# Kernel tuning notes

Measured on AMD Instinct MI355X. Metric: run time of the kernel, lower is better.

Reference implementation:

```python
import jax, jax.numpy as jnp
import numpy as np

B, S, D, H, DFF = 4, 1024, 1024, 16, 4096
DK = D // H
EPS = 1e-6


def setup_inputs() -> dict:
    key = jax.random.key(0)
    ks = jax.random.split(key, 16)
    sd = 0.02
    inp = {
        "x_v": jax.random.normal(ks[0], (B, S, D), jnp.float32),
        "x_k": jax.random.normal(ks[1], (B, S, D), jnp.float32),
        "x_q": jax.random.normal(ks[2], (B, S, D), jnp.float32),
        "mask": jnp.zeros((B, 1, S), jnp.float32),
        # per-head projections stacked: [H, D, DK]
        "wq": jax.random.normal(ks[3], (H, D, DK), jnp.float32) * sd,
        "bq": jnp.zeros((H, DK), jnp.float32),
        "wk": jax.random.normal(ks[4], (H, D, DK), jnp.float32) * sd,
        "bk": jnp.zeros((H, DK), jnp.float32),
        "wv": jax.random.normal(ks[5], (H, D, DK), jnp.float32) * sd,
        "bv": jnp.zeros((H, DK), jnp.float32),
        "w0": jax.random.normal(ks[6], (D, D), jnp.float32) * sd,
        "b0": jnp.zeros((D,), jnp.float32),
        "ln1_g": jnp.ones((D,), jnp.float32),
        "ln1_b": jnp.zeros((D,), jnp.float32),
        "ff1_w": jax.random.normal(ks[7], (D, DFF), jnp.float32) * sd,
        "ff1_b": jnp.zeros((DFF,), jnp.float32),
        "ff2_w": jax.random.normal(ks[8], (DFF, D), jnp.float32) * sd,
        "ff2_b": jnp.zeros((D,), jnp.float32),
        "ln2_g": jnp.ones((D,), jnp.float32),
        "ln2_b": jnp.zeros((D,), jnp.float32),
    }
    return inp


def layer_norm(x, g, b):
    mu = jnp.mean(x, axis=-1, keepdims=True)
    var = jnp.mean(jnp.square(x - mu), axis=-1, keepdims=True)
    return (x - mu) * jax.lax.rsqrt(var + EPS) * g + b


def reference(x_v, x_k, x_q, mask, wq, bq, wk, bk, wv, bv, w0, b0,
              ln1_g, ln1_b, ff1_w, ff1_b, ff2_w, ff2_b, ln2_g, ln2_b):
    # --- Multi-head attention (heads batched instead of Python loop) ---
    q = jnp.einsum('bsd,hdk->bhsk', x_q, wq) + bq[:, None, :]  # [B,H,S,DK]
    k = jnp.einsum('bsd,hdk->bhsk', x_k, wk) + bk[:, None, :]
    v = jnp.einsum('bsd,hdk->bhsk', x_v, wv) + bv[:, None, :]
    scores = jnp.einsum('bhqk,bhsk->bhqs', q, k) / jnp.sqrt(jnp.float32(DK))
    scores = scores + mask[:, None, :, :] * (-1e9)  # mask broadcast over heads
    attn_w = jax.nn.softmax(scores, axis=-1)        # [B,H,S,S]
    attn = jnp.einsum('bhqs,bhsk->bhqk', attn_w, v)  # [B,H,S,DK]
    concat = attn.transpose(0, 2, 1, 3).reshape(B, S, D)
    mha_out = concat @ w0 + b0
    # --- Residual + LayerNorm 1 (dropout is identity at inference) ---
    sub1 = layer_norm(x_q + mha_out, ln1_g, ln1_b)
    # --- Point-wise FFN ---
    ffn = jax.nn.relu(sub1 @ ff1_w + ff1_b) @ ff2_w + ff2_b
    # --- Residual + LayerNorm 2 ---
    out = layer_norm(sub1 + ffn, ln2_g, ln2_b)
    # original returns the attention weights of the LAST head only
    return out, attn_w[:, -1]
```

## Files before the change

kernel.cpp:

```cpp
#include <hip/hip_runtime.h>
#include <hip/hip_bf16.h>
#include <stdint.h>

#define DEV __device__ __forceinline__

typedef uint16_t u16;
typedef __attribute__((ext_vector_type(8))) short s16x8;
typedef __attribute__((ext_vector_type(8))) unsigned short u16x8;
typedef __attribute__((ext_vector_type(4))) unsigned short u16x4;
typedef __attribute__((ext_vector_type(4))) float f32x4;

constexpr int CB = 4;
constexpr int CS = 1024;
constexpr int CD = 1024;
constexpr int CH = 16;
constexpr int CDFF = 4096;
constexpr int KVB = 128;
constexpr int LSTRP = 136;
constexpr float QSCALE = 0.125f * 1.44269504f;
constexpr float MASKC  = -1.44269504e9f;

DEV float b2f(u16 u) { union { uint32_t i; float f; } v; v.i = (uint32_t)u << 16; return v.f; }
DEV u16 f2b(float f) {
  union { float f; uint32_t i; } v; v.f = f;
  uint32_t r = v.i + 0x7fffu + ((v.i >> 16) & 1u);
  return (u16)(r >> 16);
}
DEV float ex2(float x) {
#if __has_builtin(__builtin_amdgcn_exp2f)
  return __builtin_amdgcn_exp2f(x);
#else
  return __expf(x * 0.69314718056f);
#endif
}

using as1v = const __attribute__((address_space(1))) void;
using as3v = __attribute__((address_space(3))) void;
DEV void g2l16(const u16* g, u16* l) {
  __builtin_amdgcn_global_load_lds((as1v*)g, (as3v*)l, 16, 0, 0);
}

__global__ void detect_dtype(const uint32_t* __restrict__ w, uint32_t* __restrict__ flag) {
  if (threadIdx.x == 0 && blockIdx.x == 0) {
    flag[0] = (w[0] == 0x3F800000u) ? 1u : 0u;
    flag[1] = 0u;
  }
}

__global__ __launch_bounds__(256)
void cvt3(const void* __restrict__ s0, const void* __restrict__ s1, const void* __restrict__ s2,
          u16* __restrict__ d0, u16* __restrict__ d1, u16* __restrict__ d2,
          const uint32_t* __restrict__ flag)
{
  const void* s = blockIdx.z == 0 ? s0 : (blockIdx.z == 1 ? s1 : s2);
  u16* d        = blockIdx.z == 0 ? d0 : (blockIdx.z == 1 ? d1 : d2);
  size_t i = ((size_t)blockIdx.x * 256 + threadIdx.x) * 4;
  if (flag[0]) {
    const float* f = (const float*)s;
    u16x4 o;
#pragma unroll
    for (int j = 0; j < 4; j++) o[j] = f2b(f[i + j]);
    *(u16x4*)(d + i) = o;
  } else {
    *(u16x4*)(d + i) = *(const u16x4*)((const u16*)s + i);
  }
}

struct SmallCvt {
  const void* src[11];
  u16* dst[11];
  int n[11];
};
__global__ __launch_bounds__(256)
void cvt_small(SmallCvt sc, const uint32_t* __restrict__ flag)
{
  int idx = blockIdx.x * 256 + threadIdx.x;
#pragma unroll
  for (int a = 0; a < 11; a++) {
    if (idx < sc.n[a]) {
      if (flag[0]) sc.dst[a][idx] = f2b(((const float*)sc.src[a])[idx]);
      else         sc.dst[a][idx] = ((const u16*)sc.src[a])[idx];
      return;
    }
    idx -= sc.n[a];
  }
}

__global__ __launch_bounds__(256)
void transpose64d(const void* __restrict__ in, u16* __restrict__ out,
                  int in_rs, long long in_ys, long long in_zs,
                  int out_rs, long long out_ys, long long out_zs,
                  const uint32_t* __restrict__ flag)
{
  int t = blockIdx.x * 256 + threadIdx.x;
  int k  = t & 63;
  int n8 = t >> 6;
  size_t ib = (size_t)blockIdx.z * in_zs + (size_t)blockIdx.y * in_ys
            + (size_t)n8 * 8 * in_rs + k;
  u16* ob = out + (size_t)blockIdx.z * out_zs + (size_t)blockIdx.y * out_ys
                + (size_t)k * out_rs + (size_t)n8 * 8;
  u16x8 v;
  if (flag[0]) {
    const float* f = (const float*)in;
#pragma unroll
    for (int j = 0; j < 8; j++) v[j] = f2b(f[ib + (size_t)j * in_rs]);
  } else {
    const u16* u = (const u16*)in;
#pragma unroll
    for (int j = 0; j < 8; j++) v[j] = u[ib + (size_t)j * in_rs];
  }
  *(u16x8*)ob = v;
}

struct TBatch {
  const void* in[6];
  u16* out[6];
  int in_rs[6];
  long long in_ys[6];
  int out_rs[6];
  long long out_ys[6];
  int nx[6];
  int cnt[6];
};
__global__ __launch_bounds__(256)
void transpose_batch(TBatch tb, const uint32_t* __restrict__ flag)
{
  int rem = blockIdx.x;
  int e = 0;
  while (e < 5 && rem >= tb.cnt[e]) { rem -= tb.cnt[e]; e++; }
  const int bx = rem % tb.nx[e];
  const int by = rem / tb.nx[e];
  const int in_rs = tb.in_rs[e];
  int t = bx * 256 + threadIdx.x;
  int k  = t & 63;
  int n8 = t >> 6;
  size_t ib = (size_t)by * tb.in_ys[e] + (size_t)n8 * 8 * in_rs + k;
  u16* ob = tb.out[e] + (size_t)by * tb.out_ys[e] + (size_t)k * tb.out_rs[e] + (size_t)n8 * 8;
  u16x8 v;
  if (flag[0]) {
    const float* f = (const float*)tb.in[e];
#pragma unroll
    for (int j = 0; j < 8; j++) v[j] = f2b(f[ib + (size_t)j * in_rs]);
  } else {
    const u16* u = (const u16*)tb.in[e];
#pragma unroll
    for (int j = 0; j < 8; j++) v[j] = u[ib + (size_t)j * in_rs];
  }
  *(u16x8*)ob = v;
}

struct GemmArgs {
  const u16* A[3];
  const u16* Bt[3];
  const u16* bias[3];
  u16* C[3];
  float scales[3];
  int M, N, K;
  int relu;
};

template<int MI, int NI, int WGM, int WGN, int BK>
DEV void gemm_body(const GemmArgs& g)
{
  constexpr int BM = WGM * MI * 16;
  constexpr int BN = WGN * NI * 16;
  constexpr int NT = WGM * WGN * 64;
  constexpr int CPR = BK / 8;
  constexpr int CHA = BM * BK / (NT * 8);
  constexpr int CHB = BN * BK / (NT * 8);

  const int z = blockIdx.z;
  const u16* __restrict__ A    = g.A[z];
  const u16* __restrict__ Bt   = g.Bt[z];
  const u16* __restrict__ bias = g.bias[z];
  u16* __restrict__ C          = g.C[z];
  const float scale = g.scales[z];
  const int N = g.N, K = g.K;

  __shared__ __align__(16) u16 lA[BM * BK];
  __shared__ __align__(16) u16 lB[BN * BK];

  const int tid  = threadIdx.x;
  const int lane = tid & 63;
  const int wave = tid >> 6;
  const int quad = lane >> 4;
  const int l16  = lane & 15;
  const int sw   = l16 & (CPR - 1);
  const int wm = (wave / WGN) * MI * 16;
  const int wn = (wave % WGN) * NI * 16;

  const int flat = blockIdx.y * gridDim.x + blockIdx.x;
  const int nY = gridDim.y;
  const size_t bm = (size_t)(flat % nY) * BM;
  const size_t bn = (size_t)(flat / nY) * BN;

  f32x4 acc[MI][NI];
#pragma unroll
  for (int mi = 0; mi < MI; mi++)
#pragma unroll
    for (int ni = 0; ni < NI; ni++)
#pragma unroll
      for (int r = 0; r < 4; r++) acc[mi][ni][r] = 0.f;

  const u16* Ab = A + bm * K;
  const u16* Bb = Bt + bn * K;

  for (int k0 = 0; k0 < K; k0 += BK) {
#pragma unroll
    for (int i = 0; i < CHA; i++) {
      int c = i * NT + tid;
      int r = c / CPR, j = c % CPR;
      g2l16(Ab + (size_t)r * K + k0 + ((j ^ (r & (CPR - 1))) * 8), lA + c * 8);
    }
#pragma unroll
    for (int i = 0; i < CHB; i++) {
      int c = i * NT + tid;
      int r = c / CPR, j = c % CPR;
      g2l16(Bb + (size_t)r * K + k0 + ((j ^ (r & (CPR - 1))) * 8), lB + c * 8);
    }
    __syncthreads();
#pragma unroll
    for (int kk = 0; kk < BK / 32; kk++) {
      s16x8 af[MI], bfr[NI];
#pragma unroll
      for (int mi = 0; mi < MI; mi++)
        af[mi] = *(const s16x8*)(lA + (wm + mi * 16 + l16) * BK + (((kk * 4 + quad) ^ sw) * 8));
#pragma unroll
      for (int ni = 0; ni < NI; ni++)
        bfr[ni] = *(const s16x8*)(lB + (wn + ni * 16 + l16) * BK + (((kk * 4 + quad) ^ sw) * 8));
#pragma unroll
      for (int mi = 0; mi < MI; mi++)
#pragma unroll
        for (int ni = 0; ni < NI; ni++)
          acc[mi][ni] = __builtin_amdgcn_mfma_f32_16x16x32_bf16(af[mi], bfr[ni], acc[mi][ni], 0, 0, 0);
    }
    __syncthreads();
  }

  float bvals[NI];
#pragma unroll
  for (int ni = 0; ni < NI; ni++) bvals[ni] = b2f(bias[bn + wn + ni * 16 + l16]);
#pragma unroll
  for (int mi = 0; mi < MI; mi++) {
#pragma unroll
    for (int r = 0; r < 4; r++) {
      size_t row = bm + wm + mi * 16 + quad * 4 + r;
      u16* crow = C + row * N + bn + wn;
#pragma unroll
      for (int ni = 0; ni < NI; ni++) {
        float v = (acc[mi][ni][r] + bvals[ni]) * scale;
        if (g.relu) v = fmaxf(v, 0.f);
        crow[ni * 16 + l16] = f2b(v);
      }
    }
  }
}

__global__ __launch_bounds__(256, 4) void gemm_qkv (GemmArgs g) { gemm_body<4, 4, 2, 2, 64>(g); }
__global__ __launch_bounds__(128, 2) void gemm_wo  (GemmArgs g) { gemm_body<4, 2, 1, 2, 128>(g); }
__global__ __launch_bounds__(256, 4) void gemm_ffn1(GemmArgs g) { gemm_body<4, 4, 2, 2, 64>(g); }
__global__ __launch_bounds__(128, 2) void gemm_ffn2(GemmArgs g) { gemm_body<4, 2, 1, 2, 128>(g); }

__global__ __launch_bounds__(256, 3)
void flash_attn(const u16* __restrict__ Qb, const u16* __restrict__ Kb,
                const u16* __restrict__ Vt, const u16* __restrict__ mask,
                u16* __restrict__ O, float* __restrict__ ml)
{
  const int b = blockIdx.z;
  const int h = blockIdx.x & 15;
  const int q0 = (blockIdx.x >> 4) * 64;
  const int tid  = threadIdx.x;
  const int lane = tid & 63, wave = tid >> 6;
  const int quad = lane >> 4, l16 = lane & 15;
  const int sw3 = l16 & 7;
  const int sw4 = l16 & 15;

  __shared__ __align__(16) u16 lK[KVB * 64];
  __shared__ __align__(16) u16 lV[64 * KVB];
  __shared__ __align__(16) u16 lP[4][16 * LSTRP];

  s16x8 aq[2];
  {
    const u16* qp = Qb + ((size_t)b * CS + q0 + wave * 16 + l16) * CD + h * 64 + quad * 8;
    aq[0] = *(const s16x8*)qp;
    aq[1] = *(const s16x8*)(qp + 32);
  }

  f32x4 of[4];
  float m_r[4], l_r[4];
#pragma unroll
  for (int nt = 0; nt < 4; nt++)
#pragma unroll
    for (int r = 0; r < 4; r++) of[nt][r] = 0.f;
#pragma unroll
  for (int r = 0; r < 4; r++) { m_r[r] = -3.0e38f; l_r[r] = 0.f; }

  int kRow[4], kJ[4], kOff[4], vRow[4], vJ[4], vOff[4];
#pragma unroll
  for (int i = 0; i < 4; i++) {
    int c = i * 256 + tid;
    kRow[i] = c >> 3;  kJ[i] = c & 7;
    kOff[i] = kRow[i] * 64 + ((kJ[i] ^ (kRow[i] & 7)) * 8);
    vRow[i] = c >> 4;  vJ[i] = c & 15;
    vOff[i] = vRow[i] * KVB + ((vJ[i] ^ (vRow[i] & 15)) * 8);
  }

  const u16* Kbase = Kb + (size_t)b * CS * CD + h * 64;
  const u16* Vbase = Vt + ((size_t)(b * CH + h)) * 64 * CS;
  u16* lPw = lP[wave];

  u16x8 rk[4], rv[4];
#pragma unroll
  for (int i = 0; i < 4; i++) {
    rk[i] = *(const u16x8*)(Kbase + (size_t)kRow[i] * CD + kJ[i] * 8);
    rv[i] = *(const u16x8*)(Vbase + (size_t)vRow[i] * CS + vJ[i] * 8);
  }

  for (int kt = 0; kt < CS / KVB; kt++) {
    __syncthreads();
#pragma unroll
    for (int i = 0; i < 4; i++) {
      *(u16x8*)(lK + kOff[i]) = rk[i];
      *(u16x8*)(lV + vOff[i]) = rv[i];
    }
    __syncthreads();

    if (kt + 1 < CS / KVB) {
#pragma unroll
      for (int i = 0; i < 4; i++) {
        rk[i] = *(const u16x8*)(Kbase + (size_t)((kt + 1) * KVB + kRow[i]) * CD + kJ[i] * 8);
        rv[i] = *(const u16x8*)(Vbase + (size_t)vRow[i] * CS + (kt + 1) * KVB + vJ[i] * 8);
      }
    }

    f32x4 sf[8];
#pragma unroll
    for (int ni = 0; ni < 8; ni++)
#pragma unroll
      for (int r = 0; r < 4; r++) sf[ni][r] = 0.f;
#pragma unroll
    for (int kk = 0; kk < 2; kk++) {
#pragma unroll
      for (int ni = 0; ni < 8; ni++) {
        s16x8 bk = *(const s16x8*)(lK + (ni * 16 + l16) * 64 + (((kk * 4 + quad) ^ sw3) * 8));
        sf[ni] = __builtin_amdgcn_mfma_f32_16x16x32_bf16(aq[kk], bk, sf[ni], 0, 0, 0);
      }
    }
#pragma unroll
    for (int ni = 0; ni < 8; ni++) {
      float mv = b2f(mask[(size_t)b * CS + kt * KVB + ni * 16 + l16]) * MASKC;
#pragma unroll
      for (int r = 0; r < 4; r++) sf[ni][r] += mv;
    }
    float mx[4];
#pragma unroll
    for (int r = 0; r < 4; r++) {
      float a = fmaxf(fmaxf(sf[0][r], sf[1][r]), fmaxf(sf[2][r], sf[3][r]));
      float c = fmaxf(fmaxf(sf[4][r], sf[5][r]), fmaxf(sf[6][r], sf[7][r]));
      mx[r] = fmaxf(a, c);
    }
#pragma unroll
    for (int off = 1; off < 16; off <<= 1)
#pragma unroll
      for (int r = 0; r < 4; r++) mx[r] = fmaxf(mx[r], __shfl_xor(mx[r], off, 16));
    bool ng = (mx[0] <= m_r[0] + 8.f) && (mx[1] <= m_r[1] + 8.f) &&
              (mx[2] <= m_r[2] + 8.f) && (mx[3] <= m_r[3] + 8.f);
    if (!__all(ng)) {
#pragma unroll
      for (int r = 0; r < 4; r++) {
        float mn = fmaxf(m_r[r], mx[r]);
        float al = ex2(m_r[r] - mn);
        m_r[r] = mn;
        l_r[r] *= al;
#pragma unroll
        for (int nt = 0; nt < 4; nt++) of[nt][r] *= al;
      }
    }
    float ps[4] = {0.f, 0.f, 0.f, 0.f};
#pragma unroll
    for (int ni = 0; ni < 8; ni++)
#pragma unroll
      for (int r = 0; r < 4; r++) {
        float p = ex2(sf[ni][r] - m_r[r]);
        sf[ni][r] = p;
        ps[r] += p;
      }
#pragma unroll
    for (int off = 1; off < 16; off <<= 1)
#pragma unroll
      for (int r = 0; r < 4; r++) ps[r] += __shfl_xor(ps[r], off, 16);
#pragma unroll
    for (int r = 0; r < 4; r++) l_r[r] += ps[r];
#pragma unroll
    for (int ni = 0; ni < 8; ni++)
#pragma unroll
      for (int r = 0; r < 4; r++)
        lPw[(quad * 4 + r) * LSTRP + ni * 16 + l16] = f2b(sf[ni][r]);
#pragma unroll
    for (int kk = 0; kk < 4; kk++) {
      s16x8 ap = *(const s16x8*)(lPw + l16 * LSTRP + kk * 32 + quad * 8);
#pragma unroll
      for (int nt = 0; nt < 4; nt++) {
        s16x8 bv = *(const s16x8*)(lV + (nt * 16 + l16) * KVB + (((kk * 4 + quad) ^ sw4) * 8));
        of[nt] = __builtin_amdgcn_mfma_f32_16x16x32_bf16(ap, bv, of[nt], 0, 0, 0);
      }
    }
  }

#pragma unroll
  for (int r = 0; r < 4; r++) {
    float inv = 1.f / l_r[r];
    size_t row = q0 + wave * 16 + quad * 4 + r;
    u16* orow = O + ((size_t)b * CS + row) * CD + h * 64;
#pragma unroll
    for (int nt = 0; nt < 4; nt++) orow[nt * 16 + l16] = f2b(of[nt][r] * inv);
    if (h == CH - 1 && l16 == 0) {
      ml[(size_t)b * CS + row] = m_r[r];
      ml[(size_t)CB * CS + (size_t)b * CS + row] = l_r[r];
    }
  }
}

__global__ __launch_bounds__(256)
void attn_probs(const u16* __restrict__ Qb, const u16* __restrict__ Kb,
                const u16* __restrict__ mask, const float* __restrict__ ml,
                void* __restrict__ outbuf, const uint32_t* __restrict__ flag)
{
  const int b = blockIdx.z;
  const int h = CH - 1;
  const int q0 = blockIdx.x * 64;
  const int tid  = threadIdx.x;
  const int lane = tid & 63, wave = tid >> 6;
  const int quad = lane >> 4, l16 = lane & 15;
  const int sw3 = l16 & 7;
  const size_t OUT1 = (size_t)CB * CS * CD;
  const bool f32out = flag[0] != 0;

  __shared__ __align__(16) u16 lK[KVB * 64];

  s16x8 aq[2];
  {
    const u16* qp = Qb + ((size_t)b * CS + q0 + wave * 16 + l16) * CD + h * 64 + quad * 8;
    aq[0] = *(const s16x8*)qp;
    aq[1] = *(const s16x8*)(qp + 32);
  }
  float mr[4], lr[4];
#pragma unroll
  for (int r = 0; r < 4; r++) {
    size_t row = q0 + wave * 16 + quad * 4 + r;
    mr[r] = ml[(size_t)b * CS + row];
    lr[r] = 1.f / ml[(size_t)CB * CS + (size_t)b * CS + row];
  }
  int kRow[4], kJ[4], kOff[4];
#pragma unroll
  for (int i = 0; i < 4; i++) {
    int c = i * 256 + tid;
    kRow[i] = c >> 3;  kJ[i] = c & 7;
    kOff[i] = kRow[i] * 64 + ((kJ[i] ^ (kRow[i] & 7)) * 8);
  }
  const u16* Kbase = Kb + (size_t)b * CS * CD + h * 64;

  u16x8 rk[4];
#pragma unroll
  for (int i = 0; i < 4; i++)
    rk[i] = *(const u16x8*)(Kbase + (size_t)kRow[i] * CD + kJ[i] * 8);

  for (int kt = 0; kt < CS / KVB; kt++) {
    __syncthreads();
#pragma unroll
    for (int i = 0; i < 4; i++)
      *(u16x8*)(lK + kOff[i]) = rk[i];
    __syncthreads();
    if (kt + 1 < CS / KVB) {
#pragma unroll
      for (int i = 0; i < 4; i++)
        rk[i] = *(const u16x8*)(Kbase + (size_t)((kt + 1) * KVB + kRow[i]) * CD + kJ[i] * 8);
    }
    f32x4 sf[8];
#pragma unroll
    for (int ni = 0; ni < 8; ni++)
#pragma unroll
      for (int r = 0; r < 4; r++) sf[ni][r] = 0.f;
#pragma unroll
    for (int kk = 0; kk < 2; kk++) {
#pragma unroll
      for (int ni = 0; ni < 8; ni++) {
        s16x8 bk = *(const s16x8*)(lK + (ni * 16 + l16) * 64 + (((kk * 4 + quad) ^ sw3) * 8));
        sf[ni] = __builtin_amdgcn_mfma_f32_16x16x32_bf16(aq[kk], bk, sf[ni], 0, 0, 0);
      }
    }
#pragma unroll
    for (int ni = 0; ni < 8; ni++) {
      float mv = b2f(mask[(size_t)b * CS + kt * KVB + ni * 16 + l16]) * MASKC;
#pragma unroll
      for (int r = 0; r < 4; r++) {
        float p = ex2(sf[ni][r] + mv - mr[r]) * lr[r];
        size_t row = q0 + wave * 16 + quad * 4 + r;
        size_t idx = OUT1 + ((size_t)b * CS + row) * CS + kt * KVB + ni * 16 + l16;
        if (f32out) ((float*)outbuf)[idx] = p;
        else        ((u16*)outbuf)[idx] = f2b(p);
      }
    }
  }
}

__global__ __launch_bounds__(256)
void resid_ln(const u16* __restrict__ x, const u16* __restrict__ y,
              const u16* __restrict__ g, const u16* __restrict__ bb,
              void* __restrict__ out, const uint32_t* __restrict__ flag,
              int to_out)
{
  const int row = blockIdx.x;
  const int tid = threadIdx.x;
  __shared__ float rs[4], rs2[4];
  const u16* xr = x + (size_t)row * CD;
  const u16* yr = y + (size_t)row * CD;
  const int base = tid * 4;
  const bool f32out = to_out && (flag[0] != 0);
  const u16x4 xv = *(const u16x4*)(xr + base);
  const u16x4 yv = *(const u16x4*)(yr + base);
  float v[4];
  float s = 0.f, s2 = 0.f;
#pragma unroll
  for (int i = 0; i < 4; i++) {
    float a = b2f(xv[i]) + b2f(yv[i]);
    v[i] = a; s += a; s2 += a * a;
  }
#pragma unroll
  for (int off = 32; off > 0; off >>= 1) {
    s += __shfl_down(s, off, 64);
    s2 += __shfl_down(s2, off, 64);
  }
  if ((tid & 63) == 0) { rs[tid >> 6] = s; rs2[tid >> 6] = s2; }
  __syncthreads();
  float st = rs[0] + rs[1] + rs[2] + rs[3];
  float s2t = rs2[0] + rs2[1] + rs2[2] + rs2[3];
  float mu = st * (1.f / CD);
  float var = s2t * (1.f / CD) - mu * mu;
  float rstd = rsqrtf(var + 1e-6f);
  const u16x4 gv = *(const u16x4*)(g + base);
  const u16x4 bv = *(const u16x4*)(bb + base);
  float o[4];
#pragma unroll
  for (int i = 0; i < 4; i++)
    o[i] = (v[i] - mu) * rstd * b2f(gv[i]) + b2f(bv[i]);
  if (f32out) {
    f32x4 o4 = {o[0], o[1], o[2], o[3]};
    *(f32x4*)((float*)out + (size_t)row * CD + base) = o4;
  } else {
    u16x4 o4;
#pragma unroll
    for (int i = 0; i < 4; i++) o4[i] = f2b(o[i]);
    *(u16x4*)((u16*)out + (size_t)row * CD + base) = o4;
  }
}

extern "C" void kernel_launch(void* const* d_in, const int* in_sizes, int n_in,
                              void* d_out, int out_size, void* d_ws, size_t ws_size,
                              hipStream_t stream) {
  const void* x_v   = d_in[0];
  const void* x_k   = d_in[1];
  const void* x_q   = d_in[2];
  const void* maskI = d_in[3];
  const void* wq    = d_in[4];
  const void* bq    = d_in[5];
  const void* wk    = d_in[6];
  const void* bk    = d_in[7];
  const void* wv    = d_in[8];
  const void* bv    = d_in[9];
  const void* w0    = d_in[10];
  const void* b0    = d_in[11];
  const void* ln1_g = d_in[12];
  const void* ln1_b = d_in[13];
  const void* ff1_w = d_in[14];
  const void* ff1_b = d_in[15];
  const void* ff2_w = d_in[16];
  const void* ff2_b = d_in[17];
  const void* ln2_g = d_in[18];
  const void* ln2_b = d_in[19];

  u16* ws = (u16*)d_ws;
  size_t off = 0;
  auto alloc = [&](size_t n) { u16* p = ws + off; off += n; return p; };
  const size_t M1 = 1024 * 1024;
  u16* wqT   = alloc(M1);
  u16* wkT   = alloc(M1);
  u16* wvT   = alloc(M1);
  u16* w0T   = alloc(M1);
  u16* ff1T  = alloc(4 * M1);
  u16* ff2T  = alloc(4 * M1);
  u16* Qb    = alloc(4 * M1);
  u16* Kbuf  = alloc(4 * M1);
  u16* Vbuf  = alloc(4 * M1);
  u16* VtB   = alloc(4 * M1);
  u16* Ob    = alloc(4 * M1);
  u16* mha   = alloc(4 * M1);
  u16* sub1  = alloc(4 * M1);
  u16* ffmid = alloc(16 * M1);
  u16* cxq   = alloc(4 * M1);
  u16* cxk   = alloc(4 * M1);
  u16* cxv   = alloc(4 * M1);
  u16* cmask = alloc(4096);
  u16* cbq   = alloc(1024);
  u16* cbk   = alloc(1024);
  u16* cbv   = alloc(1024);
  u16* cb0   = alloc(1024);
  u16* cf1b  = alloc(4096);
  u16* cf2b  = alloc(1024);
  u16* cl1g  = alloc(1024);
  u16* cl1b  = alloc(1024);
  u16* cl2g  = alloc(1024);
  u16* cl2b  = alloc(1024);
  float* ml  = (float*)alloc(16384);
  uint32_t* flag = (uint32_t*)alloc(64);
  if (ws_size < off * sizeof(u16)) return;

  dim3 blk(256);

  detect_dtype<<<dim3(1), dim3(64), 0, stream>>>((const uint32_t*)ln1_g, flag);
  const uint32_t* fIn = flag;
  const uint32_t* fBf = flag + 1;

  cvt3<<<dim3(4096, 1, 3), blk, 0, stream>>>(x_q, x_k, x_v, cxq, cxk, cxv, fIn);
  {
    SmallCvt sc{};
    const void* s[11] = {maskI, bq, bk, bv, b0, ff1_b, ff2_b, ln1_g, ln1_b, ln2_g, ln2_b};
    u16* d[11] = {cmask, cbq, cbk, cbv, cb0, cf1b, cf2b, cl1g, cl1b, cl2g, cl2b};
    int n[11] = {4096, 1024, 1024, 1024, 1024, 4096, 1024, 1024, 1024, 1024, 1024};
    for (int i = 0; i < 11; i++) { sc.src[i] = s[i]; sc.dst[i] = d[i]; sc.n[i] = n[i]; }
    cvt_small<<<dim3(68), blk, 0, stream>>>(sc, fIn);
  }

  {
    TBatch tb{};
    const void* tin[6] = {wq, wk, wv, w0, ff1_w, ff2_w};
    u16* tout[6]       = {wqT, wkT, wvT, w0T, ff1T, ff2T};
    int irs[6]         = {64, 64, 64, CD, CDFF, CD};
    long long iys[6]   = {(long long)CD * 64, (long long)CD * 64, (long long)CD * 64, 64, 64, 64};
    int ors[6]         = {CD, CD, CD, CD, CD, CDFF};
    long long oys[6]   = {64LL * CD, 64LL * CD, 64LL * CD, 64LL * CD, 64LL * CD, 64LL * CDFF};
    int nx[6]          = {32, 32, 32, 32, 32, 128};
    int cnt[6]         = {512, 512, 512, 512, 2048, 2048};
    for (int i = 0; i < 6; i++) {
      tb.in[i] = tin[i]; tb.out[i] = tout[i];
      tb.in_rs[i] = irs[i]; tb.in_ys[i] = iys[i];
      tb.out_rs[i] = ors[i]; tb.out_ys[i] = oys[i];
      tb.nx[i] = nx[i]; tb.cnt[i] = cnt[i];
    }
    transpose_batch<<<dim3(6144), blk, 0, stream>>>(tb, fIn);
  }

  {
    GemmArgs ga{};
    ga.A[0] = cxq;  ga.A[1] = cxk;  ga.A[2] = cxv;
    ga.Bt[0] = wqT; ga.Bt[1] = wkT; ga.Bt[2] = wvT;
    ga.bias[0] = cbq; ga.bias[1] = cbk; ga.bias[2] = cbv;
    ga.C[0] = Qb; ga.C[1] = Kbuf; ga.C[2] = Vbuf;
    ga.scales[0] = QSCALE; ga.scales[1] = 1.f; ga.scales[2] = 1.f;
    ga.M = CB * CS; ga.N = CD; ga.K = CD; ga.relu = 0;
    gemm_qkv<<<dim3(8, 32, 3), blk, 0, stream>>>(ga);
  }

  transpose64d<<<dim3(32, 16, 4), blk, 0, stream>>>(Vbuf, VtB, CD, 64, (long long)CS * CD,
                                                    CS, 64LL * CS, (long long)CH * 64 * CS, fBf);

  flash_attn<<<dim3(256, 1, CB), blk, 0, stream>>>(Qb, Kbuf, VtB, cmask, Ob, ml);

  attn_probs<<<dim3(CS / 64, 1, CB), blk, 0, stream>>>(Qb, Kbuf, cmask, ml, d_out, fIn);

  {
    GemmArgs ga{};
    ga.A[0] = Ob; ga.Bt[0] = w0T; ga.bias[0] = cb0; ga.C[0] = mha;
    ga.scales[0] = 1.f;
    ga.M = CB * CS; ga.N = CD; ga.K = CD; ga.relu = 0;
    gemm_wo<<<dim3(16, 64, 1), dim3(128), 0, stream>>>(ga);
  }

  resid_ln<<<dim3(CB * CS), blk, 0, stream>>>(cxq, mha, cl1g, cl1b, sub1, fIn, 0);

  {
    GemmArgs ga{};
    ga.A[0] = sub1; ga.Bt[0] = ff1T; ga.bias[0] = cf1b; ga.C[0] = ffmid;
    ga.scales[0] = 1.f;
    ga.M = CB * CS; ga.N = CDFF; ga.K = CD; ga.relu = 1;
    gemm_ffn1<<<dim3(32, 32, 1), blk, 0, stream>>>(ga);
  }

  {
    GemmArgs ga{};
    ga.A[0] = ffmid; ga.Bt[0] = ff2T; ga.bias[0] = cf2b; ga.C[0] = mha;
    ga.scales[0] = 1.f;
    ga.M = CB * CS; ga.N = CD; ga.K = CDFF; ga.relu = 0;
    gemm_ffn2<<<dim3(16, 64, 1), dim3(128), 0, stream>>>(ga);
  }

  resid_ln<<<dim3(CB * CS), blk, 0, stream>>>(sub1, mha, cl2g, cl2b, d_out, fIn, 1);
}
```

Before: 414.2 us.

## Add double-buffered LDS GEMM body for output and FFN2 projections

Introduces a new GEMM body that stages the next K-slice into a second LDS buffer while the current one feeds the MFMA loop, so there is one barrier per iteration instead of a load-then-compute cycle. The W0 and FFN2 GEMMs switch to it with 256-thread blocks of 4 waves, each wave computing a 32x32 tile over a 64x64 block tile with BK=64, on the same grid. This aims to hide global-to-LDS latency, in exchange for smaller per-wave tiles with less register reuse and more LDS traffic per MFMA.

Measured after the change: 415.0 us (median of 2 runs). About the same (+0.2%).

```diff
diff --git a/kernel.cpp b/kernel.cpp
--- a/kernel.cpp
+++ b/kernel.cpp
@@ -256,10 +256,118 @@
   }
 }
 
+template<int MI, int NI, int WGM, int WGN, int BK>
+DEV void gemm_body_db(const GemmArgs& g)
+{
+  constexpr int BM = WGM * MI * 16;
+  constexpr int BN = WGN * NI * 16;
+  constexpr int NT = WGM * WGN * 64;
+  constexpr int CPR = BK / 8;
+  constexpr int CHA = BM * BK / (NT * 8);
+  constexpr int CHB = BN * BK / (NT * 8);
+  constexpr int HALF = (BM + BN) * BK;
+
+  const int z = blockIdx.z;
+  const u16* __restrict__ A    = g.A[z];
+  const u16* __restrict__ Bt   = g.Bt[z];
+  const u16* __restrict__ bias = g.bias[z];
+  u16* __restrict__ C          = g.C[z];
+  const float scale = g.scales[z];
+  const int N = g.N, K = g.K;
+
+  __shared__ __align__(16) u16 lds[2 * HALF];
+
+  const int tid  = threadIdx.x;
+  const int lane = tid & 63;
+  const int wave = tid >> 6;
+  const int quad = lane >> 4;
+  const int l16  = lane & 15;
+  const int sw   = l16 & (CPR - 1);
+  const int wm = (wave / WGN) * MI * 16;
+  const int wn = (wave % WGN) * NI * 16;
+
+  const int flat = blockIdx.y * gridDim.x + blockIdx.x;
+  const int nY = gridDim.y;
+  const size_t bm = (size_t)(flat % nY) * BM;
+  const size_t bn = (size_t)(flat / nY) * BN;
+
+  f32x4 acc[MI][NI];
+#pragma unroll
+  for (int mi = 0; mi < MI; mi++)
+#pragma unroll
+    for (int ni = 0; ni < NI; ni++)
+#pragma unroll
+      for (int r = 0; r < 4; r++) acc[mi][ni][r] = 0.f;
+
+  const u16* Ab = A + bm * K;
+  const u16* Bb = Bt + bn * K;
+
+  auto stage = [&](int buf, int k0) {
+    u16* sA = lds + buf * HALF;
+    u16* sB = sA + BM * BK;
+#pragma unroll
+    for (int i = 0; i < CHA; i++) {
+      int c = i * NT + tid;
+      int r = c / CPR, j = c % CPR;
+      g2l16(Ab + (size_t)r * K + k0 + ((j ^ (r & (CPR - 1))) * 8), sA + c * 8);
+    }
+#pragma unroll
+    for (int i = 0; i < CHB; i++) {
+      int c = i * NT + tid;
+      int r = c / CPR, j = c % CPR;
+      g2l16(Bb + (size_t)r * K + k0 + ((j ^ (r & (CPR - 1))) * 8), sB + c * 8);
+    }
+  };
+
+  stage(0, 0);
+  __syncthreads();
+  int cur = 0;
+  for (int k0 = 0; k0 < K; k0 += BK) {
+    if (k0 + BK < K) stage(cur ^ 1, k0 + BK);
+    const u16* lA = lds + cur * HALF;
+    const u16* lB = lA + BM * BK;
+#pragma unroll
+    for (int kk = 0; kk < BK / 32; kk++) {
+      s16x8 af[MI], bfr[NI];
+#pragma unroll
+      for (int mi = 0; mi < MI; mi++)
+        af[mi] = *(const s16x8*)(lA + (wm + mi * 16 + l16) * BK + (((kk * 4 + quad) ^ sw) * 8));
+#pragma unroll
+      for (int ni = 0; ni < NI; ni++)
+        bfr[ni] = *(const s16x8*)(lB + (wn + ni * 16 + l16) * BK + (((kk * 4 + quad) ^ sw) * 8));
+#pragma unroll
+      for (int mi = 0; mi < MI; mi++)
+#pragma unroll
+        for (int ni = 0; ni < NI; ni++)
+          acc[mi][ni] = __builtin_amdgcn_mfma_f32_16x16x32_bf16(af[mi], bfr[ni], acc[mi][ni], 0, 0, 0);
+    }
+    __syncthreads();
+    cur ^= 1;
+  }
+
+  float bvals[NI];
+#pragma unroll
+  for (int ni = 0; ni < NI; ni++) bvals[ni] = b2f(bias[bn + wn + ni * 16 + l16]);
+#pragma unroll
+  for (int mi = 0; mi < MI; mi++) {
+#pragma unroll
+    for (int r = 0; r < 4; r++) {
+      size_t row = bm + wm + mi * 16 + quad * 4 + r;
+      u16* crow = C + row * N + bn + wn;
+#pragma unroll
+      for (int ni = 0; ni < NI; ni++) {
+        float v = (acc[mi][ni][r] + bvals[ni]) * scale;
+        if (g.relu) v = fmaxf(v, 0.f);
+        crow[ni * 16 + l16] = f2b(v);
+      }
+    }
+  }
+}
+
 __global__ __launch_bounds__(256, 4) void gemm_qkv (GemmArgs g) { gemm_body<4, 4, 2, 2, 64>(g); }
-__global__ __launch_bounds__(128, 2) void gemm_wo  (GemmArgs g) { gemm_body<4, 2, 1, 2, 128>(g); }
+__global__ __launch_bounds__(256, 4) void gemm_wo  (GemmArgs g) { gemm_body_db<2, 2, 2, 2, 64>(g); }
 __global__ __launch_bounds__(256, 4) void gemm_ffn1(GemmArgs g) { gemm_body<4, 4, 2, 2, 64>(g); }
-__global__ __launch_bounds__(128, 2) void gemm_ffn2(GemmArgs g) { gemm_body<4, 2, 1, 2, 128>(g); }
+__global__ __launch_bounds__(256, 4) void gemm_ffn2(GemmArgs g) { gemm_body_db<2, 2, 2, 2, 64>(g); }
 
 __global__ __launch_bounds__(256, 3)
 void flash_attn(const u16* __restrict__ Qb, const u16* __restrict__ Kb,
@@ -673,7 +781,7 @@
     ga.A[0] = Ob; ga.Bt[0] = w0T; ga.bias[0] = cb0; ga.C[0] = mha;
     ga.scales[0] = 1.f;
     ga.M = CB * CS; ga.N = CD; ga.K = CD; ga.relu = 0;
-    gemm_wo<<<dim3(16, 64, 1), dim3(128), 0, stream>>>(ga);
+    gemm_wo<<<dim3(16, 64, 1), blk, 0, stream>>>(ga);
   }
 
   resid_ln<<<dim3(CB * CS), blk, 0, stream>>>(cxq, mha, cl1g, cl1b, sub1, fIn, 0);
@@ -691,7 +799,7 @@
     ga.A[0] = ffmid; ga.Bt[0] = ff2T; ga.bias[0] = cf2b; ga.C[0] = mha;
     ga.scales[0] = 1.f;
     ga.M = CB * CS; ga.N = CD; ga.K = CDFF; ga.relu = 0;
-    gemm_ffn2<<<dim3(16, 64, 1), dim3(128), 0, stream>>>(ga);
+    gemm_ffn2<<<dim3(16, 64, 1), blk, 0, stream>>>(ga);
   }
 
   resid_ln<<<dim3(CB * CS), blk, 0, stream>>>(sub1, mha, cl2g, cl2b, d_out, fIn, 1);
```
